# Kernel optimization log

Measured on AMD Instinct MI355X. Metric: run time of the kernel, lower is better.

The kernel has to match this reference:

```python
import jax, jax.numpy as jnp
import numpy as np

B, D, P, K, L_S = 512, 1024, 64, 16, 16


def _make_M():
    # fixed signed mask: top-left PxP block = -1, bottom-left KxP block = +1
    M = np.zeros((P + K, P + K), dtype=np.float32)
    M[:P, :P] = -1.0
    M[P:, :P] = +1.0
    return jnp.asarray(M)


def setup_inputs() -> dict:
    key = jax.random.key(0)
    k1, k2, k3 = jax.random.split(key, 3)
    X_tilde = jax.random.normal(k1, (B, D, P + K), dtype=jnp.float32)
    y_train = jax.random.normal(k2, (B, P), dtype=jnp.float32)
    gamma = jax.random.normal(k3, (D,), dtype=jnp.float32) * 0.01
    return {"X_tilde": X_tilde, "y_train": y_train, "gamma": gamma}


def reference(X_tilde, y_train, gamma):
    M = _make_M()  # [P+K, P+K]
    Bsz = X_tilde.shape[0]
    # h0 = [y_train, 0_K]  -> [B, P+K]
    h0 = jnp.concatenate([y_train, jnp.zeros((Bsz, K), dtype=y_train.dtype)], axis=-1)
    # score[b,m,n] = sum_d gamma[d] * X[b,d,m] * X[b,d,n] / P
    weighted = gamma[None, :, None] * X_tilde  # [B, D, P+K]
    score = jnp.einsum('bdm,bdn->bmn', weighted, X_tilde) / float(P)
    masked_score = M[None, :, :] * score  # [B, P+K, P+K]
    inv_L = 1.0 / float(L_S)

    def step(h, _):
        h = h + inv_L * jnp.einsum('bmn,bn->bm', masked_score, h)
        return h, None

    h, _ = jax.lax.scan(step, h0, None, length=L_S)
    return h[:, P:]
```

## Files before the change

kernel.cpp:

```cpp
#include <hip/hip_runtime.h>
#include <hip/hip_bf16.h>


namespace {
typedef __attribute__((ext_vector_type(8))) short bf16x8;
typedef __attribute__((ext_vector_type(4))) float f32x4;
typedef __attribute__((ext_vector_type(4))) float fv4;
typedef __attribute__((ext_vector_type(2))) unsigned uv2;

constexpr int kB  = 512;
constexpr int kD  = 1024;
constexpr int kP  = 64;
constexpr int kKK = 16;
constexpr int kLS = 16;
constexpr int kThreads = 320;
constexpr int kKc = 64;
constexpr int kNC = kD / kKc;

constexpr int TB    = 4096;
constexpr int ASZ   = 80 * 128;
constexpr int BSZ   = 64 * 128;
constexpr int BUFSZ = ASZ + BSZ;
constexpr int LDS_BYTES = TB + 2 * BUFSZ;
constexpr int GSTRIDE = 68;

__device__ __forceinline__ unsigned bpack(float lo, float hi) {
  __hip_bfloat16 hl = __float2bfloat16(lo);
  __hip_bfloat16 hh = __float2bfloat16(hi);
  unsigned short ul, uh;
  __builtin_memcpy(&ul, &hl, 2);
  __builtin_memcpy(&uh, &hh, 2);
  return (unsigned)ul | ((unsigned)uh << 16);
}

__global__ void __launch_bounds__(kThreads)
tcsf_kernel(const float* __restrict__ X, const float* __restrict__ y,
            const float* __restrict__ gamma, float* __restrict__ out) {
  __shared__ __align__(16) char smem[LDS_BYTES];
  float* gs = reinterpret_cast<float*>(smem);

  const int t = threadIdx.x;
  const int b = blockIdx.x;
  const int l = t & 63;
  const int w = t >> 6;

  float yv = 0.f;
  if (t < kP) yv = y[b * kP + t];
  for (int i = t; i < kD; i += kThreads) gs[i] = gamma[i];

  const fv4* Xg = reinterpret_cast<const fv4*>(X) + (size_t)b * (kD * 80 / 4);

  const int ct = t % 20;
  const int kt = t / 20;

  f32x4 acc[4];
#pragma unroll
  for (int nt = 0; nt < 4; ++nt) acc[nt] = (f32x4)(0.f);

  fv4 v0, v1, v2, v3;
  fv4 g4;

  __syncthreads();

  {
    v0 = Xg[(4 * kt) * 20 + ct];
    v1 = Xg[(4 * kt) * 20 + ct + 20];
    v2 = Xg[(4 * kt) * 20 + ct + 40];
    v3 = Xg[(4 * kt) * 20 + ct + 60];
    g4 = *reinterpret_cast<const fv4*>(gs + 4 * kt);
    char* Ab = smem + TB;
    char* Bb = Ab + ASZ;
#pragma unroll
    for (int j = 0; j < 4; ++j) {
      const int m = 4 * ct + j;
      const int off = m * 128 + ((8 * kt) ^ ((m & 7) << 4));
      uv2 wa; wa.x = bpack(v0[j], v1[j]); wa.y = bpack(v2[j], v3[j]);
      *reinterpret_cast<uv2*>(Ab + off) = wa;
      if (ct < 16) {
        uv2 wb; wb.x = bpack(g4[0] * v0[j], g4[1] * v1[j]);
        wb.y = bpack(g4[2] * v2[j], g4[3] * v3[j]);
        *reinterpret_cast<uv2*>(Bb + off) = wb;
      }
    }
  }

  const int rA = 16 * w + (l & 15);
  const int colb = (l >> 4) * 16;
  const int fswz = (l & 7) << 4;

  for (int c = 0; c < kNC; ++c) {
    if (c + 1 < kNC) {
      const int base = ((c + 1) * kKc + 4 * kt) * 20 + ct;
      v0 = Xg[base]; v1 = Xg[base + 20]; v2 = Xg[base + 40]; v3 = Xg[base + 60];
      g4 = *reinterpret_cast<const fv4*>(gs + (c + 1) * kKc + 4 * kt);
    }
    __syncthreads();
    {
      const char* Ab = smem + TB + (c & 1) * BUFSZ;
      const char* Bb = Ab + ASZ;
#pragma unroll
      for (int ks = 0; ks < 2; ++ks) {
        const int cb = ks * 64 + colb;
        const bf16x8 a = *reinterpret_cast<const bf16x8*>(Ab + rA * 128 + (cb ^ fswz));
#pragma unroll
        for (int nt = 0; nt < 4; ++nt) {
          const bf16x8 bb = *reinterpret_cast<const bf16x8*>(
              Bb + (16 * nt + (l & 15)) * 128 + (cb ^ fswz));
          acc[nt] = __builtin_amdgcn_mfma_f32_16x16x32_bf16(a, bb, acc[nt], 0, 0, 0);
        }
      }
    }
    __syncthreads();
    if (c + 1 < kNC) {
      char* Ab = smem + TB + ((c + 1) & 1) * BUFSZ;
      char* Bb = Ab + ASZ;
#pragma unroll
      for (int j = 0; j < 4; ++j) {
        const int m = 4 * ct + j;
        const int off = m * 128 + ((8 * kt) ^ ((m & 7) << 4));
        uv2 wa; wa.x = bpack(v0[j], v1[j]); wa.y = bpack(v2[j], v3[j]);
        *reinterpret_cast<uv2*>(Ab + off) = wa;
        if (ct < 16) {
          uv2 wb; wb.x = bpack(g4[0] * v0[j], g4[1] * v1[j]);
          wb.y = bpack(g4[2] * v2[j], g4[3] * v3[j]);
          *reinterpret_cast<uv2*>(Bb + off) = wb;
        }
      }
    }
  }

  float* Gl = reinterpret_cast<float*>(smem + TB);
  float* hp = Gl + 80 * GSTRIDE;
  constexpr float invP = 1.0f / 64.0f;
#pragma unroll
  for (int nt = 0; nt < 4; ++nt)
#pragma unroll
    for (int r = 0; r < 4; ++r)
      Gl[(16 * w + (l >> 4) * 4 + r) * GSTRIDE + 16 * nt + (l & 15)] =
          acc[nt][r] * invP;

  if (t < kP) hp[t] = yv;
  __syncthreads();

  const int m = t >> 2;
  const int part = t & 3;
  const fv4* Grow4 = reinterpret_cast<const fv4*>(Gl + m * GSTRIDE + part * 16);
  const fv4* hpp4  = reinterpret_cast<const fv4*>(hp + part * 16);
  const fv4 G0 = Grow4[0], G1 = Grow4[1], G2 = Grow4[2], G3 = Grow4[3];
  float hk = 0.f;
  constexpr float invL = 1.0f / kLS;
  for (int s = 0; s < kLS; ++s) {
    const fv4 h0 = hpp4[0], h1 = hpp4[1], h2 = hpp4[2], h3 = hpp4[3];
    float d0 = 0.f, d1 = 0.f, d2 = 0.f, d3 = 0.f;
#pragma unroll
    for (int i = 0; i < 4; ++i) {
      d0 = fmaf(G0[i], h0[i], d0);
      d1 = fmaf(G1[i], h1[i], d1);
      d2 = fmaf(G2[i], h2[i], d2);
      d3 = fmaf(G3[i], h3[i], d3);
    }
    float dot = (d0 + d1) + (d2 + d3);
    dot += __shfl_xor(dot, 1);
    dot += __shfl_xor(dot, 2);
    __syncthreads();
    if (part == 0) {
      if (m < kP) hp[m] -= invL * dot;
      else        hk   += invL * dot;
    }
    __syncthreads();
  }
  if (part == 0 && m >= kP) out[b * kKK + (m - kP)] = hk;
}

}

extern "C" void kernel_launch(void* const* d_in, const int* in_sizes, int n_in,
                              void* d_out, int out_size, void* d_ws, size_t ws_size,
                              hipStream_t stream) {
  const float* X     = (const float*)d_in[0];
  const float* y     = (const float*)d_in[1];
  const float* gamma = (const float*)d_in[2];
  float* out = (float*)d_out;
  tcsf_kernel<<<dim3(kB), dim3(kThreads), 0, stream>>>(X, y, gamma, out);
}
```

Measured before the change: 36.65 us.

## Deepen global-load prefetch to two chunks with register double buffering

Restructures the K-chunk loop into pairs and keeps two sets of prefetch registers. Global loads for chunks c+3 and c+4 are issued while the current chunks are staged to LDS and consumed by MFMA, so more memory latency is hidden behind compute. The cost is higher register pressure, and the staging of chunk c+1 now runs in the same barrier interval as the MFMA on buffer 0, which changes the sync pattern. Correctness depends on the two-buffer parity matching the chunk order.

```diff
diff --git a/kernel.cpp b/kernel.cpp
--- a/kernel.cpp
+++ b/kernel.cpp
@@ -33,6 +33,44 @@
   return (unsigned)ul | ((unsigned)uh << 16);
 }
 
+#define ISSUE(q, S0, S1, S2, S3)                                    \
+  { const int base_ = ((q) * kKc + 4 * kt) * 20 + ct;               \
+    S0 = Xg[base_]; S1 = Xg[base_ + 20];                            \
+    S2 = Xg[base_ + 40]; S3 = Xg[base_ + 60]; }
+
+#define STAGE(q, S0, S1, S2, S3)                                    \
+  { const fv4 g4_ = *reinterpret_cast<const fv4*>(gs + (q) * kKc + 4 * kt); \
+    char* Ab_ = smem + TB + ((q) & 1) * BUFSZ;                      \
+    char* Bb_ = Ab_ + ASZ;                                          \
+    _Pragma("unroll")                                               \
+    for (int j = 0; j < 4; ++j) {                                   \
+      const int m_ = 4 * ct + j;                                    \
+      const int off_ = m_ * 128 + ((8 * kt) ^ ((m_ & 7) << 4));     \
+      uv2 wa; wa.x = bpack(S0[j], S1[j]); wa.y = bpack(S2[j], S3[j]); \
+      *reinterpret_cast<uv2*>(Ab_ + off_) = wa;                     \
+      if (ct < 16) {                                                \
+        uv2 wb; wb.x = bpack(g4_[0] * S0[j], g4_[1] * S1[j]);       \
+        wb.y = bpack(g4_[2] * S2[j], g4_[3] * S3[j]);               \
+        *reinterpret_cast<uv2*>(Bb_ + off_) = wb;                   \
+      }                                                             \
+    } }
+
+#define MFMA_STEP(BUFPAR)                                           \
+  { const char* Ab_ = smem + TB + (BUFPAR) * BUFSZ;                 \
+    const char* Bb_ = Ab_ + ASZ;                                    \
+    _Pragma("unroll")                                               \
+    for (int ks = 0; ks < 2; ++ks) {                                \
+      const int cb_ = ks * 64 + colb;                               \
+      const bf16x8 a_ = *reinterpret_cast<const bf16x8*>(           \
+          Ab_ + rA * 128 + (cb_ ^ fswz));                           \
+      _Pragma("unroll")                                             \
+      for (int nt = 0; nt < 4; ++nt) {                              \
+        const bf16x8 bb_ = *reinterpret_cast<const bf16x8*>(        \
+            Bb_ + (16 * nt + (l & 15)) * 128 + (cb_ ^ fswz));       \
+        acc[nt] = __builtin_amdgcn_mfma_f32_16x16x32_bf16(a_, bb_, acc[nt], 0, 0, 0); \
+      }                                                             \
+    } }
+
 __global__ void __launch_bounds__(kThreads)
 tcsf_kernel(const float* __restrict__ X, const float* __restrict__ y,
             const float* __restrict__ gamma, float* __restrict__ out) {
@@ -57,77 +95,32 @@
 #pragma unroll
   for (int nt = 0; nt < 4; ++nt) acc[nt] = (f32x4)(0.f);
 
-  fv4 v0, v1, v2, v3;
-  fv4 g4;
+  fv4 sA0, sA1, sA2, sA3;
+  fv4 sB0, sB1, sB2, sB3;
 
+  ISSUE(0, sA0, sA1, sA2, sA3);
+  ISSUE(1, sB0, sB1, sB2, sB3);
   __syncthreads();
-
-  {
-    v0 = Xg[(4 * kt) * 20 + ct];
-    v1 = Xg[(4 * kt) * 20 + ct + 20];
-    v2 = Xg[(4 * kt) * 20 + ct + 40];
-    v3 = Xg[(4 * kt) * 20 + ct + 60];
-    g4 = *reinterpret_cast<const fv4*>(gs + 4 * kt);
-    char* Ab = smem + TB;
-    char* Bb = Ab + ASZ;
-#pragma unroll
-    for (int j = 0; j < 4; ++j) {
-      const int m = 4 * ct + j;
-      const int off = m * 128 + ((8 * kt) ^ ((m & 7) << 4));
-      uv2 wa; wa.x = bpack(v0[j], v1[j]); wa.y = bpack(v2[j], v3[j]);
-      *reinterpret_cast<uv2*>(Ab + off) = wa;
-      if (ct < 16) {
-        uv2 wb; wb.x = bpack(g4[0] * v0[j], g4[1] * v1[j]);
-        wb.y = bpack(g4[2] * v2[j], g4[3] * v3[j]);
-        *reinterpret_cast<uv2*>(Bb + off) = wb;
-      }
-    }
-  }
+  STAGE(0, sA0, sA1, sA2, sA3);
+  ISSUE(2, sA0, sA1, sA2, sA3);
 
   const int rA = 16 * w + (l & 15);
   const int colb = (l >> 4) * 16;
   const int fswz = (l & 7) << 4;
 
-  for (int c = 0; c < kNC; ++c) {
-    if (c + 1 < kNC) {
-      const int base = ((c + 1) * kKc + 4 * kt) * 20 + ct;
-      v0 = Xg[base]; v1 = Xg[base + 20]; v2 = Xg[base + 40]; v3 = Xg[base + 60];
-      g4 = *reinterpret_cast<const fv4*>(gs + (c + 1) * kKc + 4 * kt);
+  for (int c = 0; c < kNC; c += 2) {
+    __syncthreads();
+    STAGE(c + 1, sB0, sB1, sB2, sB3);
+    if (c + 3 < kNC) ISSUE(c + 3, sB0, sB1, sB2, sB3);
+    MFMA_STEP(0);
+    __syncthreads();
+    if (c + 2 < kNC) {
+      STAGE(c + 2, sA0, sA1, sA2, sA3);
+      if (c + 4 < kNC) ISSUE(c + 4, sA0, sA1, sA2, sA3);
     }
-    __syncthreads();
-    {
-      const char* Ab = smem + TB + (c & 1) * BUFSZ;
-      const char* Bb = Ab + ASZ;
-#pragma unroll
-      for (int ks = 0; ks < 2; ++ks) {
-        const int cb = ks * 64 + colb;
-        const bf16x8 a = *reinterpret_cast<const bf16x8*>(Ab + rA * 128 + (cb ^ fswz));
-#pragma unroll
-        for (int nt = 0; nt < 4; ++nt) {
-          const bf16x8 bb = *reinterpret_cast<const bf16x8*>(
-              Bb + (16 * nt + (l & 15)) * 128 + (cb ^ fswz));
-          acc[nt] = __builtin_amdgcn_mfma_f32_16x16x32_bf16(a, bb, acc[nt], 0, 0, 0);
-        }
-      }
-    }
-    __syncthreads();
-    if (c + 1 < kNC) {
-      char* Ab = smem + TB + ((c + 1) & 1) * BUFSZ;
-      char* Bb = Ab + ASZ;
-#pragma unroll
-      for (int j = 0; j < 4; ++j) {
-        const int m = 4 * ct + j;
-        const int off = m * 128 + ((8 * kt) ^ ((m & 7) << 4));
-        uv2 wa; wa.x = bpack(v0[j], v1[j]); wa.y = bpack(v2[j], v3[j]);
-        *reinterpret_cast<uv2*>(Ab + off) = wa;
-        if (ct < 16) {
-          uv2 wb; wb.x = bpack(g4[0] * v0[j], g4[1] * v1[j]);
-          wb.y = bpack(g4[2] * v2[j], g4[3] * v3[j]);
-          *reinterpret_cast<uv2*>(Bb + off) = wb;
-        }
-      }
-    }
+    MFMA_STEP(1);
   }
+  __syncthreads();
 
   float* Gl = reinterpret_cast<float*>(smem + TB);
   float* hp = Gl + 80 * GSTRIDE;
```

Measured after the change: 37.45 us. +2.2%, slower.
